# Kernel tuning notes

Measured on AMD Instinct MI355X. Metric: run time of the kernel, lower is better.

The kernel has to match this reference:

```python
import jax, jax.numpy as jnp
import numpy as np

S, D, H, HD, FF = 4096, 1024, 16, 64, 4096  # seq, d_embed, heads, head_dim, hidden
EPS = 1e-6  # flax LayerNorm default epsilon


def layer_norm(x, scale, bias):
    mu = jnp.mean(x, axis=-1, keepdims=True)
    var = jnp.var(x, axis=-1, keepdims=True)
    return (x - mu) * jax.lax.rsqrt(var + EPS) * scale + bias


def rope(x):
    # x: [S, H, HD]; standard half-split rotary embedding, base 10000
    half = x.shape[-1] // 2
    freq = 1.0 / (10000.0 ** (jnp.arange(half, dtype=x.dtype) / half))  # [half]
    ang = jnp.arange(x.shape[0], dtype=x.dtype)[:, None] * freq          # [S, half]
    cos = jnp.cos(ang)[:, None, :]
    sin = jnp.sin(ang)[:, None, :]
    x1, x2 = x[..., :half], x[..., half:]
    return jnp.concatenate([x1 * cos - x2 * sin, x2 * cos + x1 * sin], axis=-1)


def setup_inputs() -> dict:
    key = jax.random.key(0)
    ks = jax.random.split(key, 8)
    s = 0.02
    return {
        "x": jax.random.normal(ks[0], (S, D), jnp.float32),
        "ln1_scale": jnp.ones((D,), jnp.float32), "ln1_bias": jnp.zeros((D,), jnp.float32),
        "ln2_scale": jnp.ones((D,), jnp.float32), "ln2_bias": jnp.zeros((D,), jnp.float32),
        "Wq": jax.random.normal(ks[1], (D, H, HD), jnp.float32) * s, "bq": jnp.zeros((H, HD), jnp.float32),
        "Wk": jax.random.normal(ks[2], (D, H, HD), jnp.float32) * s, "bk": jnp.zeros((H, HD), jnp.float32),
        "Wv": jax.random.normal(ks[3], (D, H, HD), jnp.float32) * s, "bv": jnp.zeros((H, HD), jnp.float32),
        "Wo": jax.random.normal(ks[4], (H, HD, D), jnp.float32) * s, "bo": jnp.zeros((D,), jnp.float32),
        "W1": jax.random.normal(ks[5], (D, FF), jnp.float32) * s, "b1": jnp.zeros((FF,), jnp.float32),
        "W2": jax.random.normal(ks[6], (FF, D), jnp.float32) * s, "b2": jnp.zeros((D,), jnp.float32),
    }


def reference(x, ln1_scale, ln1_bias, ln2_scale, ln2_bias, Wq, bq, Wk, bk, Wv, bv, Wo, bo, W1, b1, W2, b2):
    # Pre-LN attention block with RoPE fused into QK scores
    y = layer_norm(x, ln1_scale, ln1_bias)
    q = jnp.einsum('sd,dhc->shc', y, Wq) + bq  # [S,H,HD]
    k = jnp.einsum('sd,dhc->shc', y, Wk) + bk
    v = jnp.einsum('sd,dhc->shc', y, Wv) + bv
    q = rope(q)
    k = rope(k)
    scores = jnp.einsum('qhc,khc->hqk', q, k) / jnp.sqrt(jnp.asarray(HD, x.dtype))  # [H,S,S]
    p = jax.nn.softmax(scores, axis=-1)
    o = jnp.einsum('hqk,khc->qhc', p, v)                # [S,H,HD]
    attn_out = jnp.einsum('qhc,hcd->qd', o, Wo) + bo    # [S,D]
    x = x + attn_out
    # Pre-LN GELU MLP block
    y = layer_norm(x, ln2_scale, ln2_bias)
    y = jax.nn.gelu(y @ W1 + b1, approximate=False)
    x = x + (y @ W2 + b2)
    return x
```

## Files before the change

kernel.cpp:

```cpp
#include <hip/hip_runtime.h>
#include <hip/hip_bf16.h>
#include <math.h>

using bf16 = __hip_bfloat16;
typedef __attribute__((ext_vector_type(8))) short short8;
typedef __attribute__((ext_vector_type(4))) short s16x4;
typedef __attribute__((ext_vector_type(4))) float f32x4;

constexpr int S = 4096, D = 1024, H = 16, HD = 64, FF = 4096;

static __device__ __forceinline__ float tof(bf16 v) { return __bfloat162float(v); }
static __device__ __forceinline__ bf16 tob(float v) { return __float2bfloat16(v); }
static __device__ __forceinline__ short tobs(float v) {
    bf16 h = __float2bfloat16(v);
    return *reinterpret_cast<short*>(&h);
}
static __device__ __forceinline__ unsigned pkbf16(float a, float b) {
    __hip_bfloat162 h = __float22bfloat162_rn(make_float2(a, b));
    return *reinterpret_cast<unsigned*>(&h);
}

#if __has_builtin(__builtin_amdgcn_exp2f)
#define EXP2(x) __builtin_amdgcn_exp2f(x)
#else
#define EXP2(x) exp2f(x)
#endif

static __device__ __forceinline__ f32x4 mfma16(short8 a, short8 b, f32x4 c) {
    return __builtin_amdgcn_mfma_f32_16x16x32_bf16(a, b, c, 0, 0, 0);
}
static __device__ __forceinline__ void stage16(const bf16* g, bf16* l) {
    __builtin_amdgcn_global_load_lds((__attribute__((address_space(1))) void*)g,
                                     (__attribute__((address_space(3))) void*)l, 16, 0, 0);
}
static __device__ __forceinline__ void pl32swap(unsigned& a, unsigned& b) {
    asm("v_permlane32_swap_b32 %0, %1" : "+v"(a), "+v"(b));
}
static __device__ __forceinline__ void pl16swap(unsigned& a, unsigned& b) {
    asm("v_permlane16_swap_b32 %0, %1" : "+v"(a), "+v"(b));
}

__global__ __launch_bounds__(256) void ln_kernel(const float* __restrict__ x,
                                                 const float* __restrict__ scale,
                                                 const float* __restrict__ bias,
                                                 bf16* __restrict__ y) {
    int row = blockIdx.x, t = threadIdx.x;
    const float* xr = x + (size_t)row * D;
    float v[4], s = 0.f, ss = 0.f;
#pragma unroll
    for (int i = 0; i < 4; ++i) {
        v[i] = xr[t + 256 * i];
        s += v[i]; ss += v[i] * v[i];
    }
    __shared__ float r0[256], r1[256];
    r0[t] = s; r1[t] = ss;
    __syncthreads();
    for (int off = 128; off; off >>= 1) {
        if (t < off) { r0[t] += r0[t + off]; r1[t] += r1[t + off]; }
        __syncthreads();
    }
    float mu  = r0[0] * (1.f / D);
    float var = r1[0] * (1.f / D) - mu * mu;
    float inv = rsqrtf(var + 1e-6f);
    bf16* yr = y + (size_t)row * D;
#pragma unroll
    for (int i = 0; i < 4; ++i) {
        int c = t + 256 * i;
        yr[c] = tob((v[i] - mu) * inv * scale[c] + bias[c]);
    }
}

__global__ __launch_bounds__(256) void wtrans_all(
    const float* __restrict__ Wq, const float* __restrict__ Wk,
    const float* __restrict__ Wv, const float* __restrict__ Wo,
    const float* __restrict__ W1, const float* __restrict__ W2,
    const float* __restrict__ bq, const float* __restrict__ bk,
    const float* __restrict__ bv,
    bf16* __restrict__ BTqkv, bf16* __restrict__ BTo,
    bf16* __restrict__ BT1, bf16* __restrict__ BT2, float* __restrict__ bqkv) {
    int id = blockIdx.x;
    if (id >= 12288) {
        int i = (id - 12288) * 256 + threadIdx.x;
        bqkv[i] = i < 1024 ? bq[i] : (i < 2048 ? bk[i - 1024] : bv[i - 2048]);
        return;
    }
    const float* W; bf16* dst; int K, N, local;
    if (id < 3072)      { int s = id >> 10; W = s == 0 ? Wq : (s == 1 ? Wk : Wv);
                          dst = BTqkv + (size_t)s * 1048576; K = 1024; N = 1024; local = id & 1023; }
    else if (id < 4096) { W = Wo; dst = BTo; K = 1024; N = 1024; local = id - 3072; }
    else if (id < 8192) { W = W1; dst = BT1; K = 1024; N = 4096; local = id - 4096; }
    else                { W = W2; dst = BT2; K = 4096; N = 1024; local = id - 8192; }
    int ls = (N == 4096) ? 7 : 5;
    int nt = (local & ((1 << ls) - 1)) << 5, kt = (local >> ls) << 5;
    __shared__ float t[32][33];
    int tid = threadIdx.x, r = tid >> 5, c = tid & 31;
#pragma unroll
    for (int p = 0; p < 4; ++p)
        t[r + p * 8][c] = W[(size_t)(kt + r + p * 8) * N + nt + c];
    __syncthreads();
#pragma unroll
    for (int p = 0; p < 4; ++p)
        dst[(size_t)(nt + r + p * 8) * K + kt + c] = tob(t[c][r + p * 8]);
}

#define EPI_RES  1
#define EPI_GELU 2
#define EPI_QKV  3
#define EPI_PART 4

template <int EPI, int MT>
__global__ __launch_bounds__(256, MT == 128 ? 2 : 3) void gemm_bt(
    const bf16* __restrict__ A, const bf16* __restrict__ BT,
    const float* __restrict__ bias, const float* resid, void* out, void* out2,
    int M, int N, int K, int kLen) {
    constexpr int NJ = (MT == 128) ? 4 : 2;
    __shared__ bf16 As[2][MT * 32];
    __shared__ bf16 Bs[2][128 * 32];
    const int tid = threadIdx.x;
    const int w = tid >> 6, lane = tid & 63;
    const int quad = lane >> 4, l16 = lane & 15;
    const int rowBase = blockIdx.y * MT, colBase = blockIdx.x * 128;
    const int kStart = blockIdx.z * kLen;
    const int wr = (MT == 128) ? (w >> 1) * 64 : 0;
    const int wc = (MT == 128) ? (w & 1) * 64 : w * 32;
    const int sr = lane >> 2;
    const int skb = (((lane & 3) ^ ((lane >> 3) & 3)) * 8);
    const int fr = (l16 >> 1) & 3;
    f32x4 acc[4][NJ] = {};

    auto stage = [&](int k0, int b) {
        if constexpr (MT == 128) {
#pragma unroll
            for (int t = 0; t < 2; ++t) {
                int inst = w * 2 + t;
                int r = inst * 16 + sr;
                stage16(A  + (size_t)(rowBase + r) * K + kStart + k0 + skb, &As[b][inst * 512]);
                stage16(BT + (size_t)(colBase + r) * K + kStart + k0 + skb, &Bs[b][inst * 512]);
            }
        } else {
            stage16(A + (size_t)(rowBase + w * 16 + sr) * K + kStart + k0 + skb, &As[b][w * 512]);
#pragma unroll
            for (int t = 0; t < 2; ++t) {
                int inst = w + t * 4;
                stage16(BT + (size_t)(colBase + inst * 16 + sr) * K + kStart + k0 + skb, &Bs[b][inst * 512]);
            }
        }
    };

    stage(0, 0);
    const int nSteps = kLen >> 5;
    for (int s = 0; s < nSteps; ++s) {
        const int cb = s & 1;
        __builtin_amdgcn_s_barrier();
        if (s + 1 < nSteps) {
            stage((s + 1) << 5, cb ^ 1);
            if constexpr (MT == 128) asm volatile("s_waitcnt vmcnt(4)" ::: "memory");
            else                     asm volatile("s_waitcnt vmcnt(3)" ::: "memory");
        } else {
            asm volatile("s_waitcnt vmcnt(0)" ::: "memory");
        }
        __builtin_amdgcn_s_barrier();
        const bf16* pa = &As[cb][(wr + l16) * 32 + (quad ^ fr) * 8];
        const bf16* pb = &Bs[cb][(wc + l16) * 32 + (quad ^ fr) * 8];
        short8 a[4], b[NJ];
#pragma unroll
        for (int i = 0; i < 4; ++i) a[i] = *(const short8*)(pa + i * 512);
#pragma unroll
        for (int j = 0; j < NJ; ++j) b[j] = *(const short8*)(pb + j * 512);
#pragma unroll
        for (int i = 0; i < 4; ++i)
#pragma unroll
            for (int j = 0; j < NJ; ++j) acc[i][j] = mfma16(a[i], b[j], acc[i][j]);
    }
    if (EPI == EPI_QKV) {
        bf16* QKo = (bf16*)out;
        bf16* VTo = (bf16*)out2;
        if (colBase >= 2048) {
#pragma unroll
            for (int j = 0; j < NJ; ++j) {
                int c = colBase + wc + j * 16 + l16;
                float bj = bias[c];
                size_t cc = (size_t)(c - 2048) * 4096;
#pragma unroll
                for (int i = 0; i < 4; ++i) {
                    int r0 = rowBase + wr + i * 16 + quad * 4;
                    s16x4 ov = {tobs(acc[i][j][0] + bj), tobs(acc[i][j][1] + bj),
                                tobs(acc[i][j][2] + bj), tobs(acc[i][j][3] + bj)};
                    *(s16x4*)(VTo + cc + r0) = ov;
                }
            }
        } else {
            const bool isq = colBase < 1024;
            const float qs = isq ? 0.125f * 1.44269504088896f : 1.f;
#pragma unroll
            for (int j2 = 0; j2 < 2; ++j2) {
                int dim = j2 * 16 + l16;
                float freq = __expf(-(float)dim * (9.210340371976184f / 32.f));
                int c1 = colBase + wc + j2 * 16 + l16, c2 = c1 + 32;
                float b1v = bias[c1], b2v = bias[c2];
#pragma unroll
                for (int i = 0; i < 4; ++i) {
#pragma unroll
                    for (int reg = 0; reg < 4; ++reg) {
                        int s = rowBase + wr + i * 16 + quad * 4 + reg;
                        float sn, cs;
                        sincosf((float)s * freq, &sn, &cs);
                        float x1 = acc[i][j2][reg] + b1v;
                        float x2 = acc[i][j2 + 2][reg] + b2v;
                        QKo[(size_t)s * 2048 + c1] = tob((x1 * cs - x2 * sn) * qs);
                        QKo[(size_t)s * 2048 + c2] = tob((x2 * cs + x1 * sn) * qs);
                    }
                }
            }
        }
    } else {
#pragma unroll
        for (int j = 0; j < NJ; ++j) {
            int c = colBase + wc + j * 16 + l16;
            float bj = (EPI == EPI_PART) ? 0.f : bias[c];
#pragma unroll
            for (int i = 0; i < 4; ++i) {
                int r0 = rowBase + wr + i * 16 + quad * 4;
#pragma unroll
                for (int reg = 0; reg < 4; ++reg) {
                    size_t idx = (size_t)(r0 + reg) * N + c;
                    float val = acc[i][j][reg] + bj;
                    if (EPI == EPI_RES) {
                        ((float*)out)[idx] = val + resid[idx];
                    } else if (EPI == EPI_PART) {
                        ((float*)out)[(size_t)blockIdx.z * M * N + idx] = val;
                    } else {
                        float g = 0.5f * val * (1.f + erff(val * 0.70710678118f));
                        ((bf16*)out)[idx] = tob(g);
                    }
                }
            }
        }
    }
}

__global__ __launch_bounds__(256, 4) void attn_kernel(const bf16* __restrict__ QK,
                                                      const bf16* __restrict__ VT,
                                                      float* __restrict__ Op,
                                                      float* __restrict__ lp) {
    const int bx = blockIdx.x;
    const int h = bx >> 6, qb = (bx & 63) >> 1, kh = bx & 1;
    const int w = threadIdx.x >> 6, lane = threadIdx.x & 63;
    const int quad = lane >> 4, l16 = lane & 15;
    const int q0w = qb * 128 + w * 32;
    const bf16* Qh = QK + h * 64;
    const bf16* Kh = QK + 1024 + h * 64;
    const bf16* Vh = VT + (size_t)h * 64 * 4096;

    __shared__ char smem[32768];

    const int sw = l16 & 7;
    const int rloc = lane >> 3, slot = lane & 7;
    const int schunk = (slot ^ rloc) * 8;
    const int row0 = w * 16 + rloc, row1 = w * 16 + 8 + rloc;

    short8 qf[2][2];
#pragma unroll
    for (int qt = 0; qt < 2; ++qt)
#pragma unroll
        for (int c = 0; c < 2; ++c)
            qf[qt][c] = *(const short8*)(Qh + (size_t)(q0w + qt * 16 + l16) * 2048 + c * 32 + quad * 8);

    const short ob = (l16 == 0) ? (short)0x3F80 : (short)0;
    const short8 ones8 = {ob, ob, ob, ob, ob, ob, ob, ob};

    f32x4 acc[4][2] = {};
    f32x4 accl[2] = {};
    const f32x4 zero = {0.f, 0.f, 0.f, 0.f};
    const int ktBeg = kh * 2048;

    {
        bf16* Ksb = (bf16*)smem;
        bf16* Vsb = (bf16*)(smem + 8192);
        stage16(Kh + (size_t)(ktBeg + row0) * 2048 + schunk, Ksb + w * 1024);
        stage16(Kh + (size_t)(ktBeg + row1) * 2048 + schunk, Ksb + w * 1024 + 512);
        stage16(Vh + (size_t)row0 * 4096 + ktBeg + schunk, Vsb + w * 1024);
        stage16(Vh + (size_t)row1 * 4096 + ktBeg + schunk, Vsb + w * 1024 + 512);
    }

#pragma unroll 2
    for (int t = 0; t < 32; ++t) {
        char* curb = smem + (t & 1) * 16384;
        char* nxtb = smem + ((t + 1) & 1) * 16384;
        __builtin_amdgcn_s_barrier();
        if (t < 31) {
            const int ktA = ktBeg + (t + 1) * 64;
            bf16* Ksb = (bf16*)nxtb;
            bf16* Vsb = (bf16*)(nxtb + 8192);
            stage16(Kh + (size_t)(ktA + row0) * 2048 + schunk, Ksb + w * 1024);
            stage16(Kh + (size_t)(ktA + row1) * 2048 + schunk, Ksb + w * 1024 + 512);
            stage16(Vh + (size_t)row0 * 4096 + ktA + schunk, Vsb + w * 1024);
            stage16(Vh + (size_t)row1 * 4096 + ktA + schunk, Vsb + w * 1024 + 512);
            asm volatile("s_waitcnt vmcnt(4)" ::: "memory");
        } else {
            asm volatile("s_waitcnt vmcnt(0)" ::: "memory");
        }
        __builtin_amdgcn_s_barrier();

        const bf16* Ks = (const bf16*)curb;
        const bf16* Vs = (const bf16*)(curb + 8192);

        unsigned u[4][2][2];
#pragma unroll
        for (int nt = 0; nt < 4; ++nt) {
            const bf16* kr = Ks + (nt * 16 + l16) * 64;
            short8 k0 = *(const short8*)(kr + ((quad ^ sw) * 8));
            short8 k1 = *(const short8*)(kr + (((quad + 4) ^ sw) * 8));
#pragma unroll
            for (int qt = 0; qt < 2; ++qt) {
                f32x4 st = mfma16(k1, qf[qt][1], mfma16(k0, qf[qt][0], zero));
                u[nt][qt][0] = pkbf16(EXP2(st[0]), EXP2(st[1]));
                u[nt][qt][1] = pkbf16(EXP2(st[2]), EXP2(st[3]));
            }
        }
#pragma unroll
        for (int c = 0; c < 2; ++c) {
            short8 pB[2];
#pragma unroll
            for (int qt = 0; qt < 2; ++qt) {
                unsigned a0 = u[2 * c][qt][0], a1 = u[2 * c][qt][1];
                unsigned b0 = u[2 * c + 1][qt][0], b1 = u[2 * c + 1][qt][1];
                pl32swap(a0, b0);
                pl32swap(a1, b1);
                pl16swap(a0, b0);
                pl16swap(a1, b1);
                union { unsigned u4[4]; short8 s8; } pk;
                pk.u4[0] = a0; pk.u4[1] = a1; pk.u4[2] = b0; pk.u4[3] = b1;
                pB[qt] = pk.s8;
                accl[qt] = mfma16(ones8, pB[qt], accl[qt]);
            }
#pragma unroll
            for (int vt = 0; vt < 4; ++vt) {
                short8 vf = *(const short8*)(Vs + (vt * 16 + l16) * 64 + (((c * 4 + quad) ^ sw) * 8));
#pragma unroll
                for (int qt = 0; qt < 2; ++qt)
                    acc[vt][qt] = mfma16(vf, pB[qt], acc[vt][qt]);
            }
        }
    }
    float* Oz = Op + (size_t)kh * (4096 * 1024);
#pragma unroll
    for (int qt = 0; qt < 2; ++qt) {
        int q = q0w + qt * 16 + l16;
#pragma unroll
        for (int vt = 0; vt < 4; ++vt)
            *(f32x4*)(Oz + (size_t)q * 1024 + h * 64 + vt * 16 + quad * 4) = acc[vt][qt];
        if (quad == 0) lp[kh * 65536 + h * 4096 + q] = accl[qt][0];
    }
}

__global__ __launch_bounds__(256) void merge_attn(const float* __restrict__ Op,
                                                  const float* __restrict__ lp,
                                                  bf16* __restrict__ o) {
    int i = blockIdx.x * 256 + threadIdx.x;
    int d4 = i * 4;
    int s = d4 >> 10, d = d4 & 1023, h = d >> 6;
    f32x4 a = *(const f32x4*)(Op + d4 + (size_t)s * 0);
    f32x4 b = *(const f32x4*)(Op + 4194304 + d4);
    float linv = 1.f / (lp[h * 4096 + s] + lp[65536 + h * 4096 + s]);
    s16x4 ov = {tobs(a[0] + b[0]) , 0, 0, 0};
    ov[0] = tobs((a[0] + b[0]) * linv);
    ov[1] = tobs((a[1] + b[1]) * linv);
    ov[2] = tobs((a[2] + b[2]) * linv);
    ov[3] = tobs((a[3] + b[3]) * linv);
    *(s16x4*)(o + d4) = ov;
}

__global__ __launch_bounds__(256) void merge_ffn2(const float* __restrict__ pb,
                                                  const float* __restrict__ b2,
                                                  float* __restrict__ out) {
    int i = blockIdx.x * 256 + threadIdx.x;
    int d4 = i * 4, c = d4 & 1023;
    f32x4 a = *(const f32x4*)(pb + d4);
    f32x4 b = *(const f32x4*)(pb + 4194304 + d4);
    f32x4 r = *(const f32x4*)(out + d4);
    f32x4 bb = *(const f32x4*)(b2 + c);
    f32x4 v = {a[0] + b[0] + r[0] + bb[0], a[1] + b[1] + r[1] + bb[1],
               a[2] + b[2] + r[2] + bb[2], a[3] + b[3] + r[3] + bb[3]};
    *(f32x4*)(out + d4) = v;
}

extern "C" void kernel_launch(void* const* d_in, const int* in_sizes, int n_in,
                              void* d_out, int out_size, void* d_ws, size_t ws_size,
                              hipStream_t stream) {
    const float* x   = (const float*)d_in[0];
    const float* s1  = (const float*)d_in[1];
    const float* b1n = (const float*)d_in[2];
    const float* s2  = (const float*)d_in[3];
    const float* b2n = (const float*)d_in[4];
    const float* Wq  = (const float*)d_in[5];
    const float* bq  = (const float*)d_in[6];
    const float* Wk  = (const float*)d_in[7];
    const float* bk  = (const float*)d_in[8];
    const float* Wv  = (const float*)d_in[9];
    const float* bv  = (const float*)d_in[10];
    const float* Wo  = (const float*)d_in[11];
    const float* bo  = (const float*)d_in[12];
    const float* W1  = (const float*)d_in[13];
    const float* b1  = (const float*)d_in[14];
    const float* W2  = (const float*)d_in[15];
    const float* b2  = (const float*)d_in[16];

    char* ws = (char*)d_ws;
    bf16*  y    = (bf16*)(ws);
    bf16*  QK   = (bf16*)(ws + (8ull  << 20));
    bf16*  BTo  = (bf16*)(ws + (24ull << 20));
    float* lp   = (float*)(ws + (26ull << 20));
    float* bqkv = (float*)(ws + (27ull << 20));
    bf16*  o    = (bf16*)(ws + (32ull << 20));
    bf16*  hb   = (bf16*)(ws + (40ull << 20));
    bf16*  BTqkv= (bf16*)(ws + (40ull << 20));
    float* Op   = (float*)(ws + (40ull << 20));
    bf16*  VT   = (bf16*)(ws + (72ull << 20));
    bf16*  BT1  = (bf16*)(ws + (80ull << 20));
    bf16*  BT2  = (bf16*)(ws + (88ull << 20));
    float* pb   = (float*)(ws);
    float* x1   = (float*)d_out;

    wtrans_all<<<12300, 256, 0, stream>>>(Wq, Wk, Wv, Wo, W1, W2, bq, bk, bv,
                                          BTqkv, BTo, BT1, BT2, bqkv);

    ln_kernel<<<S, 256, 0, stream>>>(x, s1, b1n, y);

    gemm_bt<EPI_QKV, 128><<<dim3(24, 32), 256, 0, stream>>>(y, BTqkv, bqkv, nullptr, QK, VT, S, 3072, D, D);

    attn_kernel<<<H * 64, 256, 0, stream>>>(QK, VT, Op, lp);
    merge_attn<<<4096, 256, 0, stream>>>(Op, lp, o);

    gemm_bt<EPI_RES, 64><<<dim3(8, 64), 256, 0, stream>>>(o, BTo, bo, x, x1, nullptr, S, D, D, D);

    ln_kernel<<<S, 256, 0, stream>>>(x1, s2, b2n, y);

    gemm_bt<EPI_GELU, 128><<<dim3(32, 32), 256, 0, stream>>>(y, BT1, b1, nullptr, hb, nullptr, S, FF, D, D);

    gemm_bt<EPI_PART, 64><<<dim3(8, 64, 2), 256, 0, stream>>>(hb, BT2, b2, nullptr, pb, nullptr, S, D, FF, 2048);
    merge_ffn2<<<4096, 256, 0, stream>>>(pb, b2, x1);
}
```

Before: 426.5 us.

## Add 256x256-tile 8-wave GEMM kernel for QKV and FFN1 projections

Adds a new GEMM kernel with 256x256 output tiles, 512 threads and a K-step of 64. It stages A and B in half-tiles into double-buffered, XOR-swizzled LDS, interleaves those global loads with four MFMA quadrants per step, raises wave priority during MFMA, and remaps block IDs to group blocks for L2 locality. The QKV (with RoPE) and GELU FFN1 launches switch to it, and the old kernel keeps only the residual and partial epilogues. The larger tile is meant to cut global and LDS traffic per FLOP, at the cost of fewer blocks (192 and 256) and higher register pressure.

```diff
diff --git a/kernel.cpp b/kernel.cpp
--- a/kernel.cpp
+++ b/kernel.cpp
@@ -103,9 +103,163 @@
         dst[(size_t)(nt + r + p * 8) * K + kt + c] = tob(t[c][r + p * 8]);
 }
 
+#define EPI_QKV  3
+#define EPI_GELU 2
+
+template <int EPI>
+__global__ __launch_bounds__(512, 2) void gemm256(
+    const bf16* __restrict__ A, const bf16* __restrict__ BT,
+    const float* __restrict__ bias, void* out, void* out2, int N, int K) {
+    __shared__ bf16 lds[2][2][2][8192];
+    const int tid = threadIdx.x;
+    const int w = tid >> 6, lane = tid & 63;
+    const int quad = lane >> 4, l16 = lane & 15;
+    const int wr = w >> 2, wn = w & 3;
+    const int gx = gridDim.x, nwg = gx * gridDim.y;
+    int bid = blockIdx.y * gx + blockIdx.x;
+    bid = (bid & 7) * (nwg >> 3) + (bid >> 3);
+    const int rowBase = (bid / gx) * 256, colBase = (bid % gx) * 256;
+
+    const int srow = lane >> 3;
+    const int schunk8 = ((lane & 7) ^ srow) * 8;
+    const int cxor = l16 & 7;
+
+    f32x4 acc[8][4] = {};
+
+    auto stageHalf = [&](int b, int mat, int h, int tk) {
+        const bf16* base = mat ? BT : A;
+        const int rb = (mat ? colBase : rowBase) + h * 128;
+#pragma unroll
+        for (int i = 0; i < 2; ++i) {
+            int r = (w * 2 + i) * 8 + srow;
+            stage16(base + (size_t)(rb + r) * K + tk * 64 + schunk8,
+                    &lds[b][mat][h][(w * 2 + i) * 512]);
+        }
+    };
+    short8 a[4][2], b0[2][2], b1[2][2];
+    auto ldA = [&](int b, int mh) {
+#pragma unroll
+        for (int mf = 0; mf < 4; ++mf)
+#pragma unroll
+            for (int s = 0; s < 2; ++s)
+                a[mf][s] = *(const short8*)&lds[b][0][wr]
+                    [(mh * 64 + mf * 16 + l16) * 64 + ((s * 4 + quad) ^ cxor) * 8];
+    };
+    auto ldB = [&](int b, int nh, short8 bb[2][2]) {
+#pragma unroll
+        for (int n2 = 0; n2 < 2; ++n2)
+#pragma unroll
+            for (int s = 0; s < 2; ++s)
+                bb[n2][s] = *(const short8*)&lds[b][1][wn >> 1]
+                    [((wn & 1) * 64 + (nh * 2 + n2) * 16 + l16) * 64 + ((s * 4 + quad) ^ cxor) * 8];
+    };
+    auto domm = [&](short8 bb[2][2], int mh, int nh) {
+        __builtin_amdgcn_s_setprio(1);
+#pragma unroll
+        for (int mf = 0; mf < 4; ++mf)
+#pragma unroll
+            for (int n2 = 0; n2 < 2; ++n2)
+#pragma unroll
+                for (int s = 0; s < 2; ++s)
+                    acc[mh * 4 + mf][nh * 2 + n2] =
+                        mfma16(a[mf][s], bb[n2][s], acc[mh * 4 + mf][nh * 2 + n2]);
+        __builtin_amdgcn_s_setprio(0);
+    };
+
+    const int nT = K >> 6;
+    stageHalf(0, 1, 0, 0); stageHalf(0, 0, 0, 0);
+    stageHalf(0, 1, 1, 0); stageHalf(0, 0, 1, 0);
+    if (nT > 1) { stageHalf(1, 1, 0, 1); stageHalf(1, 0, 0, 1); }
+
+    for (int t = 0; t < nT; ++t) {
+        const int b = t & 1, bn = b ^ 1;
+        asm volatile("" ::: "memory");
+        if (t + 1 < nT) {
+            stageHalf(bn, 1, 1, t + 1);
+            asm volatile("s_waitcnt vmcnt(6)" ::: "memory");
+        } else {
+            asm volatile("s_waitcnt vmcnt(0)" ::: "memory");
+        }
+        __builtin_amdgcn_s_barrier();
+        ldA(b, 0); ldB(b, 0, b0);
+        domm(b0, 0, 0);
+        asm volatile("" ::: "memory");
+        if (t + 1 < nT) stageHalf(bn, 0, 1, t + 1);
+        __builtin_amdgcn_s_barrier();
+        ldB(b, 1, b1);
+        domm(b1, 0, 1);
+        asm volatile("" ::: "memory");
+        if (t + 2 < nT) stageHalf(b, 1, 0, t + 2);
+        __builtin_amdgcn_s_barrier();
+        ldA(b, 1);
+        domm(b1, 1, 1);
+        asm volatile("" ::: "memory");
+        if (t + 2 < nT) stageHalf(b, 0, 0, t + 2);
+        __builtin_amdgcn_s_barrier();
+        domm(b0, 1, 0);
+    }
+
+    if (EPI == EPI_QKV) {
+        bf16* QKo = (bf16*)out;
+        bf16* VTo = (bf16*)out2;
+        if (colBase >= 2048) {
+#pragma unroll
+            for (int nf = 0; nf < 4; ++nf) {
+                int c = colBase + wn * 64 + nf * 16 + l16;
+                float bj = bias[c];
+                size_t cc = (size_t)(c - 2048) * 4096;
+#pragma unroll
+                for (int mf = 0; mf < 8; ++mf) {
+                    int r0 = rowBase + wr * 128 + mf * 16 + quad * 4;
+                    s16x4 ov = {tobs(acc[mf][nf][0] + bj), tobs(acc[mf][nf][1] + bj),
+                                tobs(acc[mf][nf][2] + bj), tobs(acc[mf][nf][3] + bj)};
+                    *(s16x4*)(VTo + cc + r0) = ov;
+                }
+            }
+        } else {
+            const bool isq = colBase < 1024;
+            const float qs = isq ? 0.125f * 1.44269504088896f : 1.f;
+#pragma unroll
+            for (int j2 = 0; j2 < 2; ++j2) {
+                int dim = j2 * 16 + l16;
+                float freq = __expf(-(float)dim * (9.210340371976184f / 32.f));
+                int c1 = colBase + wn * 64 + j2 * 16 + l16, c2 = c1 + 32;
+                float b1v = bias[c1], b2v = bias[c2];
+#pragma unroll
+                for (int mf = 0; mf < 8; ++mf) {
+#pragma unroll
+                    for (int reg = 0; reg < 4; ++reg) {
+                        int sr2 = rowBase + wr * 128 + mf * 16 + quad * 4 + reg;
+                        float sn, cs;
+                        sincosf((float)sr2 * freq, &sn, &cs);
+                        float x1 = acc[mf][j2][reg] + b1v;
+                        float x2 = acc[mf][j2 + 2][reg] + b2v;
+                        QKo[(size_t)sr2 * 2048 + c1] = tob((x1 * cs - x2 * sn) * qs);
+                        QKo[(size_t)sr2 * 2048 + c2] = tob((x2 * cs + x1 * sn) * qs);
+                    }
+                }
+            }
+        }
+    } else {
+#pragma unroll
+        for (int nf = 0; nf < 4; ++nf) {
+            int c = colBase + wn * 64 + nf * 16 + l16;
+            float bj = bias[c];
+#pragma unroll
+            for (int mf = 0; mf < 8; ++mf) {
+                int r0 = rowBase + wr * 128 + mf * 16 + quad * 4;
+#pragma unroll
+                for (int reg = 0; reg < 4; ++reg) {
+                    float val = acc[mf][nf][reg] + bj;
+                    float g = 0.5f * val * (1.f + erff(val * 0.70710678118f));
+                    ((bf16*)out)[(size_t)(r0 + reg) * N + c] = tob(g);
+                }
+            }
+        }
+    }
+}
+
 #define EPI_RES  1
-#define EPI_GELU 2
-#define EPI_QKV  3
 #define EPI_PART 4
 
 template <int EPI, int MT>
@@ -172,67 +326,21 @@
 #pragma unroll
             for (int j = 0; j < NJ; ++j) acc[i][j] = mfma16(a[i], b[j], acc[i][j]);
     }
-    if (EPI == EPI_QKV) {
-        bf16* QKo = (bf16*)out;
-        bf16* VTo = (bf16*)out2;
-        if (colBase >= 2048) {
-#pragma unroll
-            for (int j = 0; j < NJ; ++j) {
-                int c = colBase + wc + j * 16 + l16;
-                float bj = bias[c];
-                size_t cc = (size_t)(c - 2048) * 4096;
-#pragma unroll
-                for (int i = 0; i < 4; ++i) {
-                    int r0 = rowBase + wr + i * 16 + quad * 4;
-                    s16x4 ov = {tobs(acc[i][j][0] + bj), tobs(acc[i][j][1] + bj),
-                                tobs(acc[i][j][2] + bj), tobs(acc[i][j][3] + bj)};
-                    *(s16x4*)(VTo + cc + r0) = ov;
-                }
-            }
-        } else {
-            const bool isq = colBase < 1024;
-            const float qs = isq ? 0.125f * 1.44269504088896f : 1.f;
-#pragma unroll
-            for (int j2 = 0; j2 < 2; ++j2) {
-                int dim = j2 * 16 + l16;
-                float freq = __expf(-(float)dim * (9.210340371976184f / 32.f));
-                int c1 = colBase + wc + j2 * 16 + l16, c2 = c1 + 32;
-                float b1v = bias[c1], b2v = bias[c2];
-#pragma unroll
-                for (int i = 0; i < 4; ++i) {
-#pragma unroll
-                    for (int reg = 0; reg < 4; ++reg) {
-                        int s = rowBase + wr + i * 16 + quad * 4 + reg;
-                        float sn, cs;
-                        sincosf((float)s * freq, &sn, &cs);
-                        float x1 = acc[i][j2][reg] + b1v;
-                        float x2 = acc[i][j2 + 2][reg] + b2v;
-                        QKo[(size_t)s * 2048 + c1] = tob((x1 * cs - x2 * sn) * qs);
-                        QKo[(size_t)s * 2048 + c2] = tob((x2 * cs + x1 * sn) * qs);
-                    }
-                }
-            }
-        }
-    } else {
-#pragma unroll
-        for (int j = 0; j < NJ; ++j) {
-            int c = colBase + wc + j * 16 + l16;
-            float bj = (EPI == EPI_PART) ? 0.f : bias[c];
-#pragma unroll
-            for (int i = 0; i < 4; ++i) {
-                int r0 = rowBase + wr + i * 16 + quad * 4;
-#pragma unroll
-                for (int reg = 0; reg < 4; ++reg) {
-                    size_t idx = (size_t)(r0 + reg) * N + c;
-                    float val = acc[i][j][reg] + bj;
-                    if (EPI == EPI_RES) {
-                        ((float*)out)[idx] = val + resid[idx];
-                    } else if (EPI == EPI_PART) {
-                        ((float*)out)[(size_t)blockIdx.z * M * N + idx] = val;
-                    } else {
-                        float g = 0.5f * val * (1.f + erff(val * 0.70710678118f));
-                        ((bf16*)out)[idx] = tob(g);
-                    }
+#pragma unroll
+    for (int j = 0; j < NJ; ++j) {
+        int c = colBase + wc + j * 16 + l16;
+        float bj = (EPI == EPI_PART) ? 0.f : bias[c];
+#pragma unroll
+        for (int i = 0; i < 4; ++i) {
+            int r0 = rowBase + wr + i * 16 + quad * 4;
+#pragma unroll
+            for (int reg = 0; reg < 4; ++reg) {
+                size_t idx = (size_t)(r0 + reg) * N + c;
+                float val = acc[i][j][reg] + bj;
+                if (EPI == EPI_RES) {
+                    ((float*)out)[idx] = val + resid[idx];
+                } else {
+                    ((float*)out)[(size_t)blockIdx.z * M * N + idx] = val;
                 }
             }
         }
@@ -360,10 +468,10 @@
     int i = blockIdx.x * 256 + threadIdx.x;
     int d4 = i * 4;
     int s = d4 >> 10, d = d4 & 1023, h = d >> 6;
-    f32x4 a = *(const f32x4*)(Op + d4 + (size_t)s * 0);
+    f32x4 a = *(const f32x4*)(Op + d4);
     f32x4 b = *(const f32x4*)(Op + 4194304 + d4);
     float linv = 1.f / (lp[h * 4096 + s] + lp[65536 + h * 4096 + s]);
-    s16x4 ov = {tobs(a[0] + b[0]) , 0, 0, 0};
+    s16x4 ov;
     ov[0] = tobs((a[0] + b[0]) * linv);
     ov[1] = tobs((a[1] + b[1]) * linv);
     ov[2] = tobs((a[2] + b[2]) * linv);
@@ -427,7 +535,7 @@
 
     ln_kernel<<<S, 256, 0, stream>>>(x, s1, b1n, y);
 
-    gemm_bt<EPI_QKV, 128><<<dim3(24, 32), 256, 0, stream>>>(y, BTqkv, bqkv, nullptr, QK, VT, S, 3072, D, D);
+    gemm256<EPI_QKV><<<dim3(12, 16), 512, 0, stream>>>(y, BTqkv, bqkv, QK, VT, 3072, D);
 
     attn_kernel<<<H * 64, 256, 0, stream>>>(QK, VT, Op, lp);
     merge_attn<<<4096, 256, 0, stream>>>(Op, lp, o);
@@ -436,7 +544,7 @@
 
     ln_kernel<<<S, 256, 0, stream>>>(x1, s2, b2n, y);
 
-    gemm_bt<EPI_GELU, 128><<<dim3(32, 32), 256, 0, stream>>>(y, BT1, b1, nullptr, hb, nullptr, S, FF, D, D);
+    gemm256<EPI_GELU><<<dim3(16, 16), 512, 0, stream>>>(y, BT1, b1, hb, nullptr, FF, D);
 
     gemm_bt<EPI_PART, 64><<<dim3(8, 64, 2), 256, 0, stream>>>(hb, BT2, b2, nullptr, pb, nullptr, S, D, FF, 2048);
     merge_ffn2<<<4096, 256, 0, stream>>>(pb, b2, x1);
```

Measured after the change: 458.4 us. 1.07x slower.

## Drop split-K in attention and FFN2, normalize and add residual in-kernel

Applied to the files above, without the earlier changes.

The attention kernel no longer splits the key range into two halves with a separate merge pass. Each block now walks all 64 key tiles and normalizes by the row sum before writing bf16 output directly. The FFN2 GEMM also drops its two-way split-K and merge kernel and uses the residual epilogue over the full K. This removes fp32 partial buffers, two extra kernel launches and their memory traffic, but halves the grid size (512 attention blocks, 512 FFN2 blocks), which may leave CUs underused.

```diff
diff --git a/kernel.cpp b/kernel.cpp
--- a/kernel.cpp
+++ b/kernel.cpp
@@ -106,7 +106,6 @@
 #define EPI_RES  1
 #define EPI_GELU 2
 #define EPI_QKV  3
-#define EPI_PART 4
 
 template <int EPI, int MT>
 __global__ __launch_bounds__(256, MT == 128 ? 2 : 3) void gemm_bt(
@@ -217,7 +216,7 @@
 #pragma unroll
         for (int j = 0; j < NJ; ++j) {
             int c = colBase + wc + j * 16 + l16;
-            float bj = (EPI == EPI_PART) ? 0.f : bias[c];
+            float bj = bias[c];
 #pragma unroll
             for (int i = 0; i < 4; ++i) {
                 int r0 = rowBase + wr + i * 16 + quad * 4;
@@ -227,8 +226,6 @@
                     float val = acc[i][j][reg] + bj;
                     if (EPI == EPI_RES) {
                         ((float*)out)[idx] = val + resid[idx];
-                    } else if (EPI == EPI_PART) {
-                        ((float*)out)[(size_t)blockIdx.z * M * N + idx] = val;
                     } else {
                         float g = 0.5f * val * (1.f + erff(val * 0.70710678118f));
                         ((bf16*)out)[idx] = tob(g);
@@ -239,12 +236,11 @@
     }
 }
 
-__global__ __launch_bounds__(256, 4) void attn_kernel(const bf16* __restrict__ QK,
+__global__ __launch_bounds__(256, 2) void attn_kernel(const bf16* __restrict__ QK,
                                                       const bf16* __restrict__ VT,
-                                                      float* __restrict__ Op,
-                                                      float* __restrict__ lp) {
+                                                      bf16* __restrict__ o) {
     const int bx = blockIdx.x;
-    const int h = bx >> 6, qb = (bx & 63) >> 1, kh = bx & 1;
+    const int h = bx >> 5, qb = bx & 31;
     const int w = threadIdx.x >> 6, lane = threadIdx.x & 63;
     const int quad = lane >> 4, l16 = lane & 15;
     const int q0w = qb * 128 + w * 32;
@@ -272,24 +268,23 @@
     f32x4 acc[4][2] = {};
     f32x4 accl[2] = {};
     const f32x4 zero = {0.f, 0.f, 0.f, 0.f};
-    const int ktBeg = kh * 2048;
 
     {
         bf16* Ksb = (bf16*)smem;
         bf16* Vsb = (bf16*)(smem + 8192);
-        stage16(Kh + (size_t)(ktBeg + row0) * 2048 + schunk, Ksb + w * 1024);
-        stage16(Kh + (size_t)(ktBeg + row1) * 2048 + schunk, Ksb + w * 1024 + 512);
-        stage16(Vh + (size_t)row0 * 4096 + ktBeg + schunk, Vsb + w * 1024);
-        stage16(Vh + (size_t)row1 * 4096 + ktBeg + schunk, Vsb + w * 1024 + 512);
+        stage16(Kh + (size_t)row0 * 2048 + schunk, Ksb + w * 1024);
+        stage16(Kh + (size_t)row1 * 2048 + schunk, Ksb + w * 1024 + 512);
+        stage16(Vh + (size_t)row0 * 4096 + schunk, Vsb + w * 1024);
+        stage16(Vh + (size_t)row1 * 4096 + schunk, Vsb + w * 1024 + 512);
     }
 
 #pragma unroll 2
-    for (int t = 0; t < 32; ++t) {
+    for (int t = 0; t < 64; ++t) {
         char* curb = smem + (t & 1) * 16384;
         char* nxtb = smem + ((t + 1) & 1) * 16384;
         __builtin_amdgcn_s_barrier();
-        if (t < 31) {
-            const int ktA = ktBeg + (t + 1) * 64;
+        if (t < 63) {
+            const int ktA = (t + 1) * 64;
             bf16* Ksb = (bf16*)nxtb;
             bf16* Vsb = (bf16*)(nxtb + 8192);
             stage16(Kh + (size_t)(ktA + row0) * 2048 + schunk, Ksb + w * 1024);
@@ -343,46 +338,18 @@
             }
         }
     }
-    float* Oz = Op + (size_t)kh * (4096 * 1024);
 #pragma unroll
     for (int qt = 0; qt < 2; ++qt) {
+        float lq = __shfl(accl[qt][0], l16, 64);
+        float linv = 1.f / lq;
         int q = q0w + qt * 16 + l16;
 #pragma unroll
-        for (int vt = 0; vt < 4; ++vt)
-            *(f32x4*)(Oz + (size_t)q * 1024 + h * 64 + vt * 16 + quad * 4) = acc[vt][qt];
-        if (quad == 0) lp[kh * 65536 + h * 4096 + q] = accl[qt][0];
-    }
-}
-
-__global__ __launch_bounds__(256) void merge_attn(const float* __restrict__ Op,
-                                                  const float* __restrict__ lp,
-                                                  bf16* __restrict__ o) {
-    int i = blockIdx.x * 256 + threadIdx.x;
-    int d4 = i * 4;
-    int s = d4 >> 10, d = d4 & 1023, h = d >> 6;
-    f32x4 a = *(const f32x4*)(Op + d4 + (size_t)s * 0);
-    f32x4 b = *(const f32x4*)(Op + 4194304 + d4);
-    float linv = 1.f / (lp[h * 4096 + s] + lp[65536 + h * 4096 + s]);
-    s16x4 ov = {tobs(a[0] + b[0]) , 0, 0, 0};
-    ov[0] = tobs((a[0] + b[0]) * linv);
-    ov[1] = tobs((a[1] + b[1]) * linv);
-    ov[2] = tobs((a[2] + b[2]) * linv);
-    ov[3] = tobs((a[3] + b[3]) * linv);
-    *(s16x4*)(o + d4) = ov;
-}
-
-__global__ __launch_bounds__(256) void merge_ffn2(const float* __restrict__ pb,
-                                                  const float* __restrict__ b2,
-                                                  float* __restrict__ out) {
-    int i = blockIdx.x * 256 + threadIdx.x;
-    int d4 = i * 4, c = d4 & 1023;
-    f32x4 a = *(const f32x4*)(pb + d4);
-    f32x4 b = *(const f32x4*)(pb + 4194304 + d4);
-    f32x4 r = *(const f32x4*)(out + d4);
-    f32x4 bb = *(const f32x4*)(b2 + c);
-    f32x4 v = {a[0] + b[0] + r[0] + bb[0], a[1] + b[1] + r[1] + bb[1],
-               a[2] + b[2] + r[2] + bb[2], a[3] + b[3] + r[3] + bb[3]};
-    *(f32x4*)(out + d4) = v;
+        for (int vt = 0; vt < 4; ++vt) {
+            s16x4 ov = {tobs(acc[vt][qt][0] * linv), tobs(acc[vt][qt][1] * linv),
+                        tobs(acc[vt][qt][2] * linv), tobs(acc[vt][qt][3] * linv)};
+            *(s16x4*)(o + (size_t)q * 1024 + h * 64 + vt * 16 + quad * 4) = ov;
+        }
+    }
 }
 
 extern "C" void kernel_launch(void* const* d_in, const int* in_sizes, int n_in,
@@ -410,16 +377,13 @@
     bf16*  y    = (bf16*)(ws);
     bf16*  QK   = (bf16*)(ws + (8ull  << 20));
     bf16*  BTo  = (bf16*)(ws + (24ull << 20));
-    float* lp   = (float*)(ws + (26ull << 20));
     float* bqkv = (float*)(ws + (27ull << 20));
     bf16*  o    = (bf16*)(ws + (32ull << 20));
     bf16*  hb   = (bf16*)(ws + (40ull << 20));
     bf16*  BTqkv= (bf16*)(ws + (40ull << 20));
-    float* Op   = (float*)(ws + (40ull << 20));
     bf16*  VT   = (bf16*)(ws + (72ull << 20));
     bf16*  BT1  = (bf16*)(ws + (80ull << 20));
     bf16*  BT2  = (bf16*)(ws + (88ull << 20));
-    float* pb   = (float*)(ws);
     float* x1   = (float*)d_out;
 
     wtrans_all<<<12300, 256, 0, stream>>>(Wq, Wk, Wv, Wo, W1, W2, bq, bk, bv,
@@ -429,8 +393,7 @@
 
     gemm_bt<EPI_QKV, 128><<<dim3(24, 32), 256, 0, stream>>>(y, BTqkv, bqkv, nullptr, QK, VT, S, 3072, D, D);
 
-    attn_kernel<<<H * 64, 256, 0, stream>>>(QK, VT, Op, lp);
-    merge_attn<<<4096, 256, 0, stream>>>(Op, lp, o);
+    attn_kernel<<<H * 32, 256, 0, stream>>>(QK, VT, o);
 
     gemm_bt<EPI_RES, 64><<<dim3(8, 64), 256, 0, stream>>>(o, BTo, bo, x, x1, nullptr, S, D, D, D);
 
@@ -438,6 +401,5 @@
 
     gemm_bt<EPI_GELU, 128><<<dim3(32, 32), 256, 0, stream>>>(y, BT1, b1, nullptr, hb, nullptr, S, FF, D, D);
 
-    gemm_bt<EPI_PART, 64><<<dim3(8, 64, 2), 256, 0, stream>>>(hb, BT2, b2, nullptr, pb, nullptr, S, D, FF, 2048);
-    merge_ffn2<<<4096, 256, 0, stream>>>(pb, b2, x1);
-}
+    gemm_bt<EPI_RES, 64><<<dim3(8, 64), 256, 0, stream>>>(hb, BT2, b2, x1, x1, nullptr, S, D, FF, FF);
+}
```

Result: faster. 409.5 us (-4.0%).
